# Kernel optimization log

Measured on AMD Instinct MI355X. Metric: run time of the kernel, lower is better.

## Reference

```python
import jax, jax.numpy as jnp
import numpy as np

NUM_LOC = 20000
T = 24
IN_DIM = 18
H1 = 32
H2 = 32
GRU = 32
PW = 15
E_RAND = 640000


def setup_inputs() -> dict:
    key = jax.random.key(0)
    ks = jax.random.split(key, 32)
    # graph: random edges + self loops so every node has >=1 incoming edge
    edge_src = jnp.concatenate([
        jax.random.randint(ks[0], (E_RAND,), 0, NUM_LOC),
        jnp.arange(NUM_LOC)]).astype(jnp.int32)
    edge_dst = jnp.concatenate([
        jax.random.randint(ks[1], (E_RAND,), 0, NUM_LOC),
        jnp.arange(NUM_LOC)]).astype(jnp.int32)
    dynamic = jax.random.normal(ks[2], (NUM_LOC, T, IN_DIM), dtype=jnp.float32)
    cI = jax.random.uniform(ks[3], (T,), dtype=jnp.float32)
    cR = jax.random.uniform(ks[4], (T,), dtype=jnp.float32)
    I = jax.random.uniform(ks[5], (T,), dtype=jnp.float32)
    R = jax.random.uniform(ks[6], (T,), dtype=jnp.float32)
    N = jax.random.uniform(ks[7], (NUM_LOC, 1), dtype=jnp.float32) * 1e4 + 10.0
    h0 = jax.random.normal(ks[8], (1, GRU), dtype=jnp.float32) * 0.1
    s = 0.1
    # GAT layer 1 (torch Linear convention: weight [out, in], y = x @ W.T + b)
    W1 = jax.random.normal(ks[9], (H1, IN_DIM), dtype=jnp.float32) * s
    b1 = jnp.zeros((H1,), dtype=jnp.float32)
    aW1 = jax.random.normal(ks[10], (1, 2 * H1), dtype=jnp.float32) * s
    ab1 = jnp.zeros((1,), dtype=jnp.float32)
    # GAT layer 2
    W2 = jax.random.normal(ks[11], (H2, H1), dtype=jnp.float32) * s
    b2 = jnp.zeros((H2,), dtype=jnp.float32)
    aW2 = jax.random.normal(ks[12], (1, 2 * H2), dtype=jnp.float32) * s
    ab2 = jnp.zeros((1,), dtype=jnp.float32)
    # GRUCell
    Wih = jax.random.normal(ks[13], (3 * GRU, H2), dtype=jnp.float32) * s
    Whh = jax.random.normal(ks[14], (3 * GRU, GRU), dtype=jnp.float32) * s
    bih = jnp.zeros((3 * GRU,), dtype=jnp.float32)
    bhh = jnp.zeros((3 * GRU,), dtype=jnp.float32)
    # output heads
    WI = jax.random.normal(ks[15], (PW, GRU + 2), dtype=jnp.float32) * s
    bI = jnp.zeros((PW,), dtype=jnp.float32)
    WR = jax.random.normal(ks[16], (PW, GRU + 2), dtype=jnp.float32) * s
    bR = jnp.zeros((PW,), dtype=jnp.float32)
    Ws = jax.random.normal(ks[17], (2, GRU + 2), dtype=jnp.float32) * s
    bs = jnp.zeros((2,), dtype=jnp.float32)
    return {"dynamic": dynamic, "cI": cI, "cR": cR, "N": N, "I": I, "R": R,
            "h0": h0, "W1": W1, "b1": b1, "aW1": aW1, "ab1": ab1,
            "W2": W2, "b2": b2, "aW2": aW2, "ab2": ab2,
            "Wih": Wih, "Whh": Whh, "bih": bih, "bhh": bhh,
            "WI": WI, "bI": bI, "WR": WR, "bR": bR, "Ws": Ws, "bs": bs,
            "edge_src": edge_src, "edge_dst": edge_dst}


def _gat(x, W, b, aW, ab, src, dst):
    # z = fc(x); per-edge attention e = leaky_relu(attn_fc([z_src, z_dst]))
    z = x @ W.T + b                                        # [n, out]
    e = jax.nn.leaky_relu(
        (jnp.concatenate([z[src], z[dst]], axis=1) @ aW.T + ab)[:, 0])  # [E]
    # softmax over incoming edges per destination node
    m = jax.ops.segment_max(e, dst, num_segments=NUM_LOC)
    ex = jnp.exp(e - m[dst])
    den = jax.ops.segment_sum(ex, dst, num_segments=NUM_LOC)
    alpha = ex / den[dst]
    return jax.ops.segment_sum(alpha[:, None] * z[src], dst, num_segments=NUM_LOC)


def reference(dynamic, cI, cR, N, I, R, h0,
              W1, b1, aW1, ab1, W2, b2, aW2, ab2,
              Wih, Whh, bih, bhh, WI, bI, WR, bR, Ws, bs,
              edge_src, edge_dst):
    Nv = N[:, 0]                                          # [num_loc]

    def step(h, inp):
        x_t, cI_t, cR_t, I_t, R_t = inp
        c = jax.nn.elu(_gat(x_t, W1, b1, aW1, ab1, edge_src, edge_dst))
        c = jax.nn.elu(_gat(c, W2, b2, aW2, ab2, edge_src, edge_dst))
        pooled = jnp.max(c, axis=0)[None, :]              # [1, H2]
        # GRUCell
        gi = pooled @ Wih.T + bih
        gh = h @ Whh.T + bhh
        r = jax.nn.sigmoid(gi[:, :GRU] + gh[:, :GRU])
        zg = jax.nn.sigmoid(gi[:, GRU:2 * GRU] + gh[:, GRU:2 * GRU])
        n = jnp.tanh(gi[:, 2 * GRU:] + r * gh[:, 2 * GRU:])
        h_new = (1.0 - zg) * n + zg * h                   # [1, GRU]
        hc = jnp.concatenate([h_new, cI_t.reshape(1, 1), cR_t.reshape(1, 1)], axis=1)
        pred_I = hc @ WI.T + bI                           # [1, PW]
        pred_R = hc @ WR.T + bR
        sir = hc @ Ws.T + bs                              # [1, 2]
        alpha = jax.nn.sigmoid(sir[0, 0])
        beta = jax.nn.sigmoid(sir[0, 1])

        def sir_step(carry, _):
            lI, lR = carry
            lS = Nv - lI - lR
            dI = alpha * lI * (lS / Nv) - beta * lI
            dR = beta * lI
            return (lI + jax.lax.stop_gradient(dI),
                    lR + jax.lax.stop_gradient(dR)), (dI, dR)

        init = (jnp.broadcast_to(I_t, Nv.shape), jnp.broadcast_to(R_t, Nv.shape))
        _, (dIs, dRs) = jax.lax.scan(sir_step, init, None, length=PW)
        # [PW, num_loc] -> [num_loc, PW]
        return h_new, (pred_I, pred_R, dIs.T, dRs.T)

    xs = (jnp.swapaxes(dynamic, 0, 1), cI, cR, I, R)      # time-major
    h_fin, (nI, nR, pI, pR) = jax.lax.scan(step, h0, xs)
    new_I = jnp.transpose(nI, (1, 0, 2))                  # [1, T, PW]
    new_R = jnp.transpose(nR, (1, 0, 2))
    phy_I = jnp.transpose(pI, (1, 0, 2))                  # [num_loc, T, PW]
    phy_R = jnp.transpose(pR, (1, 0, 2))
    return new_I, new_R, phy_I, phy_R, h_fin
```

## Files before the change

### kernel.cpp

```cpp
#include <hip/hip_runtime.h>
#include <hip/hip_fp16.h>
#include <math.h>
#include <float.h>

#define NLOC 20000
#define TT   24
#define INDIM 18
#define HH   32
#define PWN  15
#define PSTR 32

typedef unsigned short u16;

__device__ __forceinline__ unsigned int fkey(float f) {
    unsigned int b = __float_as_uint(f);
    return b ^ ((unsigned int)((int)b >> 31) | 0x80000000u);
}
__device__ __forceinline__ float funkey(unsigned int u) {
    return (u & 0x80000000u) ? __uint_as_float(u ^ 0x80000000u) : __uint_as_float(~u);
}

__device__ __forceinline__ void decode_t(int nblk, int swz, int tadd,
                                         int& t, int& blk, int& slice) {
    if (swz) {
        int F = blockIdx.x;
        int k = F & 7;
        int g = F >> 3;
        t = k + 8 * (g / nblk);
        blk = g % nblk;
        slice = t;
    } else {
        slice = blockIdx.y;
        t = tadd + slice;
        blk = blockIdx.x;
    }
}

__global__ void count_kernel(const int* __restrict__ dst, int* __restrict__ cnt, int E) {
    int e = blockIdx.x * blockDim.x + threadIdx.x;
    if (e < E) atomicAdd(&cnt[dst[e]], 1);
}

__global__ void scan_kernel(const int* __restrict__ cnt, int* __restrict__ row_ptr, int n) {
    __shared__ int sums[1024];
    const int CH = 20;
    int tid = threadIdx.x;
    int base = tid * CH;
    int local[CH];
    int s = 0;
    #pragma unroll
    for (int i = 0; i < CH; ++i) {
        int idx = base + i;
        int v = (idx < n) ? cnt[idx] : 0;
        local[i] = s;
        s += v;
    }
    sums[tid] = s;
    __syncthreads();
    for (int o = 1; o < 1024; o <<= 1) {
        int v = (tid >= o) ? sums[tid - o] : 0;
        __syncthreads();
        sums[tid] += v;
        __syncthreads();
    }
    int pre = (tid > 0) ? sums[tid - 1] : 0;
    #pragma unroll
    for (int i = 0; i < CH; ++i) {
        int idx = base + i;
        if (idx < n) row_ptr[idx] = pre + local[i];
    }
    if (tid == 1023) row_ptr[n] = sums[1023];
}

__global__ void scatter_kernel(const int* __restrict__ src, const int* __restrict__ dst,
                               const int* __restrict__ row_ptr, int* __restrict__ fill,
                               u16* __restrict__ csr_src, int E) {
    int e = blockIdx.x * blockDim.x + threadIdx.x;
    if (e < E) {
        int d = dst[e];
        int pos = row_ptr[d] + atomicAdd(&fill[d], 1);
        csr_src[pos] = (u16)src[e];
    }
}

template<int IN, bool XABS, typename TIN>
__global__ void node_kernel(const TIN* __restrict__ xbase, long nstride, long tstride,
                            const float* __restrict__ W, const float* __restrict__ b,
                            const float* __restrict__ aW, const float* __restrict__ ab,
                            __half* __restrict__ z, float* __restrict__ es, float* __restrict__ ed,
                            int nblk, int swz, int tadd) {
    __shared__ float sW[HH * IN];
    __shared__ float sb[HH];
    __shared__ float saW[2 * HH];
    __shared__ float sab;
    int t, blk, slice;
    decode_t(nblk, swz, tadd, t, blk, slice);
    int tid = threadIdx.x;
    for (int i = tid; i < HH * IN; i += blockDim.x) sW[i] = W[i];
    if (tid < HH) sb[tid] = b[tid];
    if (tid < 2 * HH) saW[tid] = aW[tid];
    if (tid == 0) sab = ab[0];
    __syncthreads();
    int n = blk * blockDim.x + tid;
    if (n >= NLOC) return;
    z  += (size_t)slice * NLOC * HH;
    es += (size_t)slice * NLOC;
    ed += (size_t)slice * NLOC;
    long xoff = XABS ? (long)t * tstride : (long)slice * tstride;
    const TIN* xp = xbase + (long)n * nstride + xoff;
    float xr[IN];
    #pragma unroll
    for (int i = 0; i < IN; ++i) xr[i] = (float)xp[i];
    float e_s = 0.f, e_d = sab;
    #pragma unroll
    for (int k = 0; k < HH; ++k) {
        float acc = sb[k];
        #pragma unroll
        for (int i = 0; i < IN; ++i) acc = fmaf(xr[i], sW[k * IN + i], acc);
        z[n * HH + k] = __float2half_rn(acc);
        e_s = fmaf(saW[k], acc, e_s);
        e_d = fmaf(saW[HH + k], acc, e_d);
    }
    es[n] = e_s;
    ed[n] = e_d;
}

template<bool WRITE_C, bool POOL>
__global__ void __launch_bounds__(256, 4)
agg_kernel(const int* __restrict__ row_ptr, const u16* __restrict__ csr,
           const __half* __restrict__ zt, const float* __restrict__ es,
           const float* __restrict__ ed, __half* __restrict__ cout,
           unsigned int* __restrict__ pooled_u, int nblk, int swz, int tadd) {
    __shared__ int2  shp[4][64];
    __shared__ float sred[4][HH];
    int t, dblk, slice;
    decode_t(nblk, swz, tadd, t, dblk, slice);
    int lane = threadIdx.x & 63;
    int w    = threadIdx.x >> 6;
    int j    = lane & 31;
    int hv   = lane >> 5;
    int d = dblk * 4 + w;
    const __half* z   = zt + (size_t)slice * NLOC * HH;
    const float*  est = es + (size_t)slice * NLOC;
    const float*  edt = ed + (size_t)slice * NLOC;

    int beg = 0, end = 0;
    float edd = 0.f;
    if (d < NLOC) {
        beg = row_ptr[d];
        end = row_ptr[d + 1];
        edd = edt[d];
    }
    int il = beg + lane;
    bool valid = (il < end);
    int idx_l = valid ? (int)csr[il] : 0;
    float ev = est[idx_l] + edd;
    ev = (ev > 0.f) ? ev : 0.01f * ev;
    float w_l = valid ? __expf(ev) : 0.f;
    float den = w_l;
    #pragma unroll
    for (int o = 32; o; o >>= 1) den += __shfl_xor(den, o, 64);
    shp[w][lane] = make_int2(idx_l, __float_as_int(w_l));
    __syncthreads();
    float acc0 = 0.f, acc1 = 0.f, acc2 = 0.f, acc3 = 0.f;
    #pragma unroll
    for (int c = 0; c < 64; c += 16) {
        int2 pr[8];
        float zr[8];
        #pragma unroll
        for (int k2 = 0; k2 < 8; ++k2) pr[k2] = shp[w][c + 2 * k2 + hv];
        #pragma unroll
        for (int k2 = 0; k2 < 8; ++k2) zr[k2] = __half2float(z[(size_t)pr[k2].x * HH + j]);
        acc0 = fmaf(__int_as_float(pr[0].y), zr[0], acc0);
        acc1 = fmaf(__int_as_float(pr[1].y), zr[1], acc1);
        acc2 = fmaf(__int_as_float(pr[2].y), zr[2], acc2);
        acc3 = fmaf(__int_as_float(pr[3].y), zr[3], acc3);
        acc0 = fmaf(__int_as_float(pr[4].y), zr[4], acc0);
        acc1 = fmaf(__int_as_float(pr[5].y), zr[5], acc1);
        acc2 = fmaf(__int_as_float(pr[6].y), zr[6], acc2);
        acc3 = fmaf(__int_as_float(pr[7].y), zr[7], acc3);
    }
    float acc = (acc0 + acc1) + (acc2 + acc3);
    float dent = 0.f;
    for (int i = beg + 64 + hv; i < end; i += 2) {
        int s2 = (int)csr[i];
        float ee = est[s2] + edd;
        ee = (ee > 0.f) ? ee : 0.01f * ee;
        float xx = __expf(ee);
        dent += xx;
        acc = fmaf(xx, __half2float(z[(size_t)s2 * HH + j]), acc);
    }
    acc  += __shfl_xor(acc, 32, 64);
    dent += __shfl_xor(dent, 32, 64);
    den  += dent;

    float cval = -FLT_MAX;
    if (d < NLOC) {
        float v = acc / den;
        cval = (v > 0.f) ? v : expm1f(v);
        if (WRITE_C && hv == 0)
            cout[(size_t)slice * NLOC * HH + (size_t)d * HH + j] = __float2half_rn(cval);
    }
    if (POOL) {
        if (hv == 0) sred[w][j] = cval;
        __syncthreads();
        if (threadIdx.x < HH) {
            float m = fmaxf(fmaxf(sred[0][threadIdx.x], sred[1][threadIdx.x]),
                            fmaxf(sred[2][threadIdx.x], sred[3][threadIdx.x]));
            atomicMax(&pooled_u[(size_t)(t * HH + threadIdx.x) * PSTR], fkey(m));
        }
    }
}

__global__ void gru_all_kernel(const unsigned int* __restrict__ pooled_u,
                               const float* __restrict__ Wih, const float* __restrict__ Whh,
                               const float* __restrict__ bih, const float* __restrict__ bhh,
                               const float* __restrict__ WI, const float* __restrict__ bI,
                               const float* __restrict__ WR, const float* __restrict__ bR,
                               const float* __restrict__ Ws, const float* __restrict__ bs,
                               const float* __restrict__ cIv, const float* __restrict__ cRv,
                               const float* __restrict__ h0, float* __restrict__ abArr,
                               float* __restrict__ out_newI, float* __restrict__ out_newR,
                               float* __restrict__ h_fin) {
    __shared__ float pooled[HH], hs[HH], gi[96], gh[96], hc[34];
    int tid = threadIdx.x;
    float wih_r[HH], whh_r[HH];
    if (tid < 96) {
        #pragma unroll
        for (int k = 0; k < HH; ++k) {
            wih_r[k] = Wih[tid * HH + k];
            whh_r[k] = Whh[tid * HH + k];
        }
    }
    if (tid < HH) hs[tid] = h0[tid];
    __syncthreads();
    for (int t = 0; t < TT; ++t) {
        if (tid < HH) pooled[tid] = funkey(pooled_u[(size_t)(t * HH + tid) * PSTR]);
        __syncthreads();
        if (tid < 96) {
            float a = bih[tid], g = bhh[tid];
            #pragma unroll
            for (int k = 0; k < HH; ++k) {
                a = fmaf(wih_r[k], pooled[k], a);
                g = fmaf(whh_r[k], hs[k], g);
            }
            gi[tid] = a; gh[tid] = g;
        }
        __syncthreads();
        if (tid < HH) {
            float r  = 1.f / (1.f + expf(-(gi[tid] + gh[tid])));
            float zg = 1.f / (1.f + expf(-(gi[HH + tid] + gh[HH + tid])));
            float nn = tanhf(gi[2 * HH + tid] + r * gh[2 * HH + tid]);
            float hn = (1.f - zg) * nn + zg * hs[tid];
            hs[tid] = hn;
            hc[tid] = hn;
        }
        if (tid == 32) hc[32] = cIv[t];
        if (tid == 33) hc[33] = cRv[t];
        __syncthreads();
        if (tid < PWN) {
            float a = bI[tid];
            #pragma unroll
            for (int k = 0; k < 34; ++k) a = fmaf(WI[tid * 34 + k], hc[k], a);
            out_newI[t * PWN + tid] = a;
        } else if (tid >= 32 && tid < 32 + PWN) {
            int p = tid - 32;
            float a = bR[p];
            #pragma unroll
            for (int k = 0; k < 34; ++k) a = fmaf(WR[p * 34 + k], hc[k], a);
            out_newR[t * PWN + p] = a;
        } else if (tid == 64 || tid == 65) {
            int p = tid - 64;
            float a = bs[p];
            #pragma unroll
            for (int k = 0; k < 34; ++k) a = fmaf(Ws[p * 34 + k], hc[k], a);
            abArr[2 * t + p] = 1.f / (1.f + expf(-a));
        }
        __syncthreads();
    }
    if (tid < HH) h_fin[tid] = hs[tid];
}

__global__ void sir_kernel(const float* __restrict__ Nin, const float* __restrict__ Iv,
                           const float* __restrict__ Rv, const float* __restrict__ abArr,
                           float* __restrict__ phyI, float* __restrict__ phyR) {
    int idx = blockIdx.x * blockDim.x + threadIdx.x;
    if (idx >= NLOC * TT) return;
    int n = idx / TT, t = idx - n * TT;
    float Nv = Nin[n];
    float alpha = abArr[2 * t], beta = abArr[2 * t + 1];
    float lI = Iv[t], lR = Rv[t];
    float* oI = phyI + (size_t)idx * PWN;
    float* oR = phyR + (size_t)idx * PWN;
    #pragma unroll
    for (int p = 0; p < PWN; ++p) {
        float lS = Nv - lI - lR;
        float dI = alpha * lI * (lS / Nv) - beta * lI;
        float dR = beta * lI;
        oI[p] = dI;
        oR[p] = dR;
        lI += dI;
        lR += dR;
    }
}

extern "C" void kernel_launch(void* const* d_in, const int* in_sizes, int n_in,
                              void* d_out, int out_size, void* d_ws, size_t ws_size,
                              hipStream_t stream) {
    const float* dynamic = (const float*)d_in[0];
    const float* cIv = (const float*)d_in[1];
    const float* cRv = (const float*)d_in[2];
    const float* Nin = (const float*)d_in[3];
    const float* Iv  = (const float*)d_in[4];
    const float* Rv  = (const float*)d_in[5];
    const float* h0  = (const float*)d_in[6];
    const float* W1  = (const float*)d_in[7];
    const float* b1  = (const float*)d_in[8];
    const float* aW1 = (const float*)d_in[9];
    const float* ab1 = (const float*)d_in[10];
    const float* W2  = (const float*)d_in[11];
    const float* b2  = (const float*)d_in[12];
    const float* aW2 = (const float*)d_in[13];
    const float* ab2 = (const float*)d_in[14];
    const float* Wih = (const float*)d_in[15];
    const float* Whh = (const float*)d_in[16];
    const float* bih = (const float*)d_in[17];
    const float* bhh = (const float*)d_in[18];
    const float* WI  = (const float*)d_in[19];
    const float* bI  = (const float*)d_in[20];
    const float* WR  = (const float*)d_in[21];
    const float* bR  = (const float*)d_in[22];
    const float* Ws  = (const float*)d_in[23];
    const float* bs  = (const float*)d_in[24];
    const int* esrc  = (const int*)d_in[25];
    const int* edst  = (const int*)d_in[26];
    const int E = in_sizes[25];

    float* out = (float*)d_out;
    float* out_newI = out;
    float* out_newR = out + TT * PWN;
    float* phyI = out + 2 * TT * PWN;
    float* phyR = phyI + (size_t)NLOC * TT * PWN;
    float* h_fin = phyR + (size_t)NLOC * TT * PWN;

    char* p = (char*)d_ws;
    int* cnt = (int*)p;                 p += (size_t)NLOC * 4;
    int* fill = (int*)p;                p += (size_t)NLOC * 4;
    int* row_ptr = (int*)p;             p += (size_t)(NLOC + 2) * 4;
    u16* csr = (u16*)p;                 p += ((size_t)E * 2 + 3) & ~(size_t)3;
    unsigned int* pooled_u = (unsigned int*)p; p += (size_t)TT * HH * PSTR * 4;
    float* abArr = (float*)p;           p += (size_t)2 * TT * 4;
    size_t fixed_bytes = (size_t)(p - (char*)d_ws);
    size_t per_t_bytes = (size_t)(2 * NLOC * HH * 2 + 2 * NLOC * 4);
    int B = 1;
    if (ws_size > fixed_bytes + per_t_bytes)
        B = (int)((ws_size - fixed_bytes) / per_t_bytes);
    if (B > TT) B = TT;
    if (B < 1) B = 1;
    __half* zb  = (__half*)p;
    __half* cb  = zb + (size_t)B * NLOC * HH;
    float* esb  = (float*)(cb + (size_t)B * NLOC * HH);
    float* edb  = esb + (size_t)B * NLOC;

    hipMemsetAsync(cnt, 0, (size_t)2 * NLOC * 4, stream);
    hipMemsetAsync(pooled_u, 0, (size_t)TT * HH * PSTR * 4, stream);

    int egrid = (E + 255) / 256;
    count_kernel<<<egrid, 256, 0, stream>>>(edst, cnt, E);
    scan_kernel<<<1, 1024, 0, stream>>>(cnt, row_ptr, NLOC);
    scatter_kernel<<<egrid, 256, 0, stream>>>(esrc, edst, row_ptr, fill, csr, E);

    const int NBLK_N = (NLOC + 255) / 256;
    const int NBLK_A = (NLOC + 3) / 4;

    if (B >= TT) {
        dim3 ng(NBLK_N * TT), ag(NBLK_A * TT);
        node_kernel<INDIM, true, float><<<ng, 256, 0, stream>>>(
            dynamic, (long)TT * INDIM, (long)INDIM, W1, b1, aW1, ab1,
            zb, esb, edb, NBLK_N, 1, 0);
        agg_kernel<true, false><<<ag, 256, 0, stream>>>(
            row_ptr, csr, zb, esb, edb, cb, pooled_u, NBLK_A, 1, 0);
        node_kernel<HH, false, __half><<<ng, 256, 0, stream>>>(
            cb, (long)HH, (long)NLOC * HH, W2, b2, aW2, ab2,
            zb, esb, edb, NBLK_N, 1, 0);
        agg_kernel<false, true><<<ag, 256, 0, stream>>>(
            row_ptr, csr, zb, esb, edb, nullptr, pooled_u, NBLK_A, 1, 0);
    } else {
        for (int tbase = 0; tbase < TT; tbase += B) {
            int Bc = TT - tbase; if (Bc > B) Bc = B;
            dim3 ng(NBLK_N, Bc), ag(NBLK_A, Bc);
            node_kernel<INDIM, true, float><<<ng, 256, 0, stream>>>(
                dynamic, (long)TT * INDIM, (long)INDIM, W1, b1, aW1, ab1,
                zb, esb, edb, NBLK_N, 0, tbase);
            agg_kernel<true, false><<<ag, 256, 0, stream>>>(
                row_ptr, csr, zb, esb, edb, cb, pooled_u, NBLK_A, 0, tbase);
            node_kernel<HH, false, __half><<<ng, 256, 0, stream>>>(
                cb, (long)HH, (long)NLOC * HH, W2, b2, aW2, ab2,
                zb, esb, edb, NBLK_N, 0, tbase);
            agg_kernel<false, true><<<ag, 256, 0, stream>>>(
                row_ptr, csr, zb, esb, edb, nullptr, pooled_u, NBLK_A, 0, tbase);
        }
    }

    gru_all_kernel<<<1, 128, 0, stream>>>(pooled_u, Wih, Whh, bih, bhh,
                                          WI, bI, WR, bR, Ws, bs, cIv, cRv,
                                          h0, abArr, out_newI, out_newR, h_fin);
    sir_kernel<<<(NLOC * TT + 255) / 256, 256, 0, stream>>>(Nin, Iv, Rv, abArr, phyI, phyR);
}
```

Before: 761.2 us.

## Vectorize GAT aggregation gathers: 8 edges per wave, 4 features per lane

The aggregation kernel's wave mapping changes from 2 edges × 32 scalar features to 8 edges × 8 lanes, each lane loading 4 half features through two half2 loads. Partial sums are then combined with xor shuffles across edge groups. The output is written as packed 8-byte stores, the half-precision input load in the projection kernel is vectorized with half2, and workspace buffers are aligned to 16 bytes so the vector accesses are valid. The aim is fewer, wider memory transactions on the random neighbor gathers, at the cost of extra shuffle reductions.

```diff
diff --git a/kernel.cpp b/kernel.cpp
--- a/kernel.cpp
+++ b/kernel.cpp
@@ -2,6 +2,7 @@
 #include <hip/hip_fp16.h>
 #include <math.h>
 #include <float.h>
+#include <type_traits>
 
 #define NLOC 20000
 #define TT   24
@@ -109,8 +110,17 @@
     long xoff = XABS ? (long)t * tstride : (long)slice * tstride;
     const TIN* xp = xbase + (long)n * nstride + xoff;
     float xr[IN];
-    #pragma unroll
-    for (int i = 0; i < IN; ++i) xr[i] = (float)xp[i];
+    if constexpr (std::is_same<TIN, __half>::value) {
+        const __half2* hp = (const __half2*)xp;
+        #pragma unroll
+        for (int i = 0; i < IN / 2; ++i) {
+            float2 f = __half22float2(hp[i]);
+            xr[2 * i] = f.x; xr[2 * i + 1] = f.y;
+        }
+    } else {
+        #pragma unroll
+        for (int i = 0; i < IN; ++i) xr[i] = (float)xp[i];
+    }
     float e_s = 0.f, e_d = sab;
     #pragma unroll
     for (int k = 0; k < HH; ++k) {
@@ -137,8 +147,8 @@
     decode_t(nblk, swz, tadd, t, dblk, slice);
     int lane = threadIdx.x & 63;
     int w    = threadIdx.x >> 6;
-    int j    = lane & 31;
-    int hv   = lane >> 5;
+    int r    = lane >> 3;
+    int cg   = lane & 7;
     int d = dblk * 4 + w;
     const __half* z   = zt + (size_t)slice * NLOC * HH;
     const float*  est = es + (size_t)slice * NLOC;
@@ -151,6 +161,7 @@
         end = row_ptr[d + 1];
         edd = edt[d];
     }
+    int deg = end - beg;
     int il = beg + lane;
     bool valid = (il < end);
     int idx_l = valid ? (int)csr[il] : 0;
@@ -162,47 +173,66 @@
     for (int o = 32; o; o >>= 1) den += __shfl_xor(den, o, 64);
     shp[w][lane] = make_int2(idx_l, __float_as_int(w_l));
     __syncthreads();
-    float acc0 = 0.f, acc1 = 0.f, acc2 = 0.f, acc3 = 0.f;
-    #pragma unroll
-    for (int c = 0; c < 64; c += 16) {
-        int2 pr[8];
-        float zr[8];
-        #pragma unroll
-        for (int k2 = 0; k2 < 8; ++k2) pr[k2] = shp[w][c + 2 * k2 + hv];
-        #pragma unroll
-        for (int k2 = 0; k2 < 8; ++k2) zr[k2] = __half2float(z[(size_t)pr[k2].x * HH + j]);
-        acc0 = fmaf(__int_as_float(pr[0].y), zr[0], acc0);
-        acc1 = fmaf(__int_as_float(pr[1].y), zr[1], acc1);
-        acc2 = fmaf(__int_as_float(pr[2].y), zr[2], acc2);
-        acc3 = fmaf(__int_as_float(pr[3].y), zr[3], acc3);
-        acc0 = fmaf(__int_as_float(pr[4].y), zr[4], acc0);
-        acc1 = fmaf(__int_as_float(pr[5].y), zr[5], acc1);
-        acc2 = fmaf(__int_as_float(pr[6].y), zr[6], acc2);
-        acc3 = fmaf(__int_as_float(pr[7].y), zr[7], acc3);
-    }
-    float acc = (acc0 + acc1) + (acc2 + acc3);
+
+    float a0 = 0.f, a1 = 0.f, a2 = 0.f, a3 = 0.f;
+    #pragma unroll
+    for (int pass = 0; pass < 8; ++pass) {
+        int2 pw = shp[w][pass * 8 + r];
+        float we = __int_as_float(pw.y);
+        const __half2* zp = (const __half2*)(z + (size_t)pw.x * HH + cg * 4);
+        __half2 h01 = zp[0], h23 = zp[1];
+        a0 = fmaf(we, __half2float(__low2half(h01)),  a0);
+        a1 = fmaf(we, __half2float(__high2half(h01)), a1);
+        a2 = fmaf(we, __half2float(__low2half(h23)),  a2);
+        a3 = fmaf(we, __half2float(__high2half(h23)), a3);
+    }
     float dent = 0.f;
-    for (int i = beg + 64 + hv; i < end; i += 2) {
-        int s2 = (int)csr[i];
+    for (int e = 64 + r; e < deg; e += 8) {
+        int s2 = (int)csr[beg + e];
         float ee = est[s2] + edd;
         ee = (ee > 0.f) ? ee : 0.01f * ee;
         float xx = __expf(ee);
         dent += xx;
-        acc = fmaf(xx, __half2float(z[(size_t)s2 * HH + j]), acc);
-    }
-    acc  += __shfl_xor(acc, 32, 64);
-    dent += __shfl_xor(dent, 32, 64);
-    den  += dent;
-
-    float cval = -FLT_MAX;
+        const __half2* zp = (const __half2*)(z + (size_t)s2 * HH + cg * 4);
+        __half2 h01 = zp[0], h23 = zp[1];
+        a0 = fmaf(xx, __half2float(__low2half(h01)),  a0);
+        a1 = fmaf(xx, __half2float(__high2half(h01)), a1);
+        a2 = fmaf(xx, __half2float(__low2half(h23)),  a2);
+        a3 = fmaf(xx, __half2float(__high2half(h23)), a3);
+    }
+    #pragma unroll
+    for (int o = 8; o <= 32; o <<= 1) {
+        a0 += __shfl_xor(a0, o, 64);
+        a1 += __shfl_xor(a1, o, 64);
+        a2 += __shfl_xor(a2, o, 64);
+        a3 += __shfl_xor(a3, o, 64);
+        dent += __shfl_xor(dent, o, 64);
+    }
+    den += dent;
+
+    float v0 = -FLT_MAX, v1 = -FLT_MAX, v2 = -FLT_MAX, v3 = -FLT_MAX;
     if (d < NLOC) {
-        float v = acc / den;
-        cval = (v > 0.f) ? v : expm1f(v);
-        if (WRITE_C && hv == 0)
-            cout[(size_t)slice * NLOC * HH + (size_t)d * HH + j] = __float2half_rn(cval);
+        float rden = 1.f / den;
+        v0 = a0 * rden; v0 = (v0 > 0.f) ? v0 : expm1f(v0);
+        v1 = a1 * rden; v1 = (v1 > 0.f) ? v1 : expm1f(v1);
+        v2 = a2 * rden; v2 = (v2 > 0.f) ? v2 : expm1f(v2);
+        v3 = a3 * rden; v3 = (v3 > 0.f) ? v3 : expm1f(v3);
+        if (WRITE_C && r == 0) {
+            __half2 o01 = __floats2half2_rn(v0, v1);
+            __half2 o23 = __floats2half2_rn(v2, v3);
+            uint2 pk;
+            pk.x = *(unsigned int*)&o01;
+            pk.y = *(unsigned int*)&o23;
+            *(uint2*)&cout[(size_t)slice * NLOC * HH + (size_t)d * HH + cg * 4] = pk;
+        }
     }
     if (POOL) {
-        if (hv == 0) sred[w][j] = cval;
+        if (r == 0) {
+            sred[w][cg * 4 + 0] = v0;
+            sred[w][cg * 4 + 1] = v1;
+            sred[w][cg * 4 + 2] = v2;
+            sred[w][cg * 4 + 3] = v3;
+        }
         __syncthreads();
         if (threadIdx.x < HH) {
             float m = fmaxf(fmaxf(sred[0][threadIdx.x], sred[1][threadIdx.x]),
@@ -347,9 +377,10 @@
     int* cnt = (int*)p;                 p += (size_t)NLOC * 4;
     int* fill = (int*)p;                p += (size_t)NLOC * 4;
     int* row_ptr = (int*)p;             p += (size_t)(NLOC + 2) * 4;
-    u16* csr = (u16*)p;                 p += ((size_t)E * 2 + 3) & ~(size_t)3;
+    u16* csr = (u16*)p;                 p += ((size_t)E * 2 + 15) & ~(size_t)15;
     unsigned int* pooled_u = (unsigned int*)p; p += (size_t)TT * HH * PSTR * 4;
     float* abArr = (float*)p;           p += (size_t)2 * TT * 4;
+    p = (char*)(((size_t)p + 15) & ~(size_t)15);
     size_t fixed_bytes = (size_t)(p - (char*)d_ws);
     size_t per_t_bytes = (size_t)(2 * NLOC * HH * 2 + 2 * NLOC * 4);
     int B = 1;
```

After: 749.4 us. About the same (-1.6%).
